# Performance work log

Hardware: AMD Instinct MI355X
Metric: run time of the kernel (lower is better)

The kernel has to match this reference:

```python
import jax, jax.numpy as jnp
import numpy as np

EPS = 1e-8  # torch cosine_similarity norm clamp

def _cos(a, b, axis=-1):
    na = jnp.maximum(jnp.linalg.norm(a, axis=axis), EPS)
    nb = jnp.maximum(jnp.linalg.norm(b, axis=axis), EPS)
    return jnp.sum(a * b, axis=axis) / (na * nb)

def setup_inputs() -> dict:
    key = jax.random.key(0)
    ks = jax.random.split(key, 9)
    B, L, D, S = 8, 8192, 512, 131072
    scale = 0.02
    x = jax.random.normal(ks[0], (B, L, D), jnp.float32)
    context_W = jax.random.normal(ks[1], (D, D), jnp.float32) * scale
    context_b = jnp.zeros((D,), jnp.float32)
    pred_W1 = jax.random.normal(ks[2], (D, D), jnp.float32) * scale
    pred_b1 = jnp.zeros((D,), jnp.float32)
    pred_W2 = jax.random.normal(ks[3], (D, D), jnp.float32) * scale
    pred_b2 = jnp.zeros((D,), jnp.float32)
    raw_embeddings = jax.random.normal(ks[4], (S, D), jnp.float32)
    u = jax.random.uniform(ks[5], (S,), jnp.float32)
    surprise_level = jnp.where(u > 0.5, u, 0.0)  # ~half the slots active
    return {"x": x, "context_W": context_W, "context_b": context_b,
            "pred_W1": pred_W1, "pred_b1": pred_b1,
            "pred_W2": pred_W2, "pred_b2": pred_b2,
            "raw_embeddings": raw_embeddings, "surprise_level": surprise_level}

def reference(x, context_W, context_b, pred_W1, pred_b1, pred_W2, pred_b2,
              raw_embeddings, surprise_level):
    # context = pad(x[:, :-1], left-shift by one along seq), i.e. causal previous token
    context = jnp.pad(x[:, :-1, :], ((0, 0), (1, 0), (0, 0)))
    # predictor MLP on projected context (torch Linear: y = x @ W.T + b)
    ctx = context @ context_W.T + context_b
    h = jax.nn.gelu(ctx @ pred_W1.T + pred_b1, approximate=False)
    prediction = h @ pred_W2.T + pred_b2  # [B, L, D]
    mse = jnp.mean((x - prediction) ** 2, axis=-1)
    prediction_surprise = jnp.sqrt(mse)  # [B, L]

    # memory-contrastive surprise: cosine sim of pooled x vs active stored embeddings
    active = surprise_level > 0  # [S]
    x_pooled = jnp.mean(x, axis=1)  # [B, D]
    sim = _cos(x_pooled[:, None, :], raw_embeddings[None, :, :])  # [B, S]
    sim = jnp.where(active[None, :], sim, -jnp.inf)
    max_sim = jnp.max(sim, axis=-1)           # [B]
    best_idx = jnp.argmax(sim, axis=-1)       # [B]
    best_stored = raw_embeddings[best_idx]    # [B, D] argmax-based gather
    divergence = 1.0 - _cos(x, best_stored[:, None, :])  # [B, L]
    pattern_match = (max_sim[:, None] > 0.3).astype(x.dtype)
    contrastive = pattern_match * divergence

    surprise = jnp.maximum(prediction_surprise, contrastive * 2.0)  # [B, L]
    return surprise
```

## Files before the change

### kernel.cpp

```cpp
#include <hip/hip_runtime.h>
#include <math.h>

#define OFF_SIMKEY   0
#define OFF_POOLED   1024
#define ZEROED_BYTES 17408
#define OFF_MAXSIM   17408
#define OFF_NORME    17664
#define OFF_EBEST    17920
#define OFF_BPRIME   34304
#define OFF_WP       36864
#define OFF_W2B      561152

typedef __attribute__((ext_vector_type(8))) short bf16x8;
typedef __attribute__((ext_vector_type(4))) float f32x4;

__device__ inline unsigned short f2bf(float f) {
    unsigned int u = __float_as_uint(f);
    unsigned int r = (u + 0x7FFFu + ((u >> 16) & 1u)) >> 16;
    return (unsigned short)r;
}

__global__ void __launch_bounds__(256) k_pre(const float* __restrict__ W1, const float* __restrict__ Wc,
                      const float* __restrict__ b1, const float* __restrict__ bc,
                      unsigned short* __restrict__ Wp, float* __restrict__ bprime) {
    __shared__ float w1row[512];
    __shared__ float wsum[4];
    int t = threadIdx.x;
    int n = blockIdx.x >> 1, half = blockIdx.x & 1;
    if (t < 128) ((float4*)w1row)[t] = ((const float4*)(W1 + (size_t)n * 512))[t];
    __syncthreads();
    int k = half * 256 + t;
    float acc = 0.f;
#pragma unroll 8
    for (int j = 0; j < 512; ++j) acc += w1row[j] * Wc[(size_t)j * 512 + k];
    Wp[(size_t)n * 512 + k] = f2bf(acc);
    if (half == 0) {
        float p = w1row[t] * bc[t] + w1row[t + 256] * bc[t + 256];
#pragma unroll
        for (int m = 32; m >= 1; m >>= 1) p += __shfl_xor(p, m);
        if ((t & 63) == 0) wsum[t >> 6] = p;
        __syncthreads();
        if (t == 0) bprime[n] = b1[n] + wsum[0] + wsum[1] + wsum[2] + wsum[3];
    }
}

__global__ void __launch_bounds__(256) k_cast(const float* __restrict__ W2, unsigned short* __restrict__ W2b) {
    int i = blockIdx.x * 1024 + threadIdx.x * 4;
    float4 v = *(const float4*)(W2 + i);
    ushort4 o;
    o.x = f2bf(v.x); o.y = f2bf(v.y); o.z = f2bf(v.z); o.w = f2bf(v.w);
    *(ushort4*)(W2b + i) = o;
}

__global__ void __launch_bounds__(512) k_pool(const float* __restrict__ x, float* __restrict__ pooled) {
    __shared__ float4 pb[4][128];
    int t = threadIdx.x;
    int q = t & 127;
    int rg = t >> 7;
    int b = blockIdx.y;
    int l0 = blockIdx.x * 128;
    const float4* p = (const float4*)(x + ((size_t)b * 8192 + l0 + rg) * 512) + q;
    float4 s = make_float4(0.f, 0.f, 0.f, 0.f);
#pragma unroll 8
    for (int i = 0; i < 32; ++i) {
        float4 v = p[(size_t)i * 512];
        s.x += v.x; s.y += v.y; s.z += v.z; s.w += v.w;
    }
    pb[rg][q] = s;
    __syncthreads();
    if (rg == 0) {
        float4 a = pb[0][q], b1_ = pb[1][q], c = pb[2][q], d = pb[3][q];
        atomicAdd(&pooled[b * 512 + q * 4 + 0], a.x + b1_.x + c.x + d.x);
        atomicAdd(&pooled[b * 512 + q * 4 + 1], a.y + b1_.y + c.y + d.y);
        atomicAdd(&pooled[b * 512 + q * 4 + 2], a.z + b1_.z + c.z + d.z);
        atomicAdd(&pooled[b * 512 + q * 4 + 3], a.w + b1_.w + c.w + d.w);
    }
}

__global__ void __launch_bounds__(256) k_sim(const float* __restrict__ E, const float* __restrict__ sl,
                     const float* __restrict__ pooledws, unsigned long long* __restrict__ simkey) {
    __shared__ float ps[4096];
    __shared__ unsigned long long wkey[4][8];
    int t = threadIdx.x, lane = t & 63, w = t >> 6;
#pragma unroll
    for (int c = 0; c < 16; ++c) ps[t + c * 256] = pooledws[t + c * 256] * (1.0f / 8192.0f);
    __syncthreads();
    float pr[8][8];
#pragma unroll
    for (int b = 0; b < 8; ++b) {
        float4 v0 = *(const float4*)&ps[b * 512 + lane * 8];
        float4 v1 = *(const float4*)&ps[b * 512 + lane * 8 + 4];
        pr[b][0] = v0.x; pr[b][1] = v0.y; pr[b][2] = v0.z; pr[b][3] = v0.w;
        pr[b][4] = v1.x; pr[b][5] = v1.y; pr[b][6] = v1.z; pr[b][7] = v1.w;
    }
    float npinv[8];
#pragma unroll
    for (int b = 0; b < 8; ++b) {
        float s = 0.f;
#pragma unroll
        for (int j = 0; j < 8; ++j) s += pr[b][j] * pr[b][j];
#pragma unroll
        for (int m = 32; m >= 1; m >>= 1) s += __shfl_xor(s, m);
        npinv[b] = 1.0f / fmaxf(sqrtf(s), 1e-8f);
    }
    unsigned long long best[8];
#pragma unroll
    for (int b = 0; b < 8; ++b) best[b] = 0ull;
    int sbase = blockIdx.x * 64 + w * 16;
    float mysl = (lane < 16) ? sl[sbase + lane] : 0.f;
    unsigned long long mask = __ballot(mysl > 0.0f);
    for (int it = 0; it < 16; ++it) {
        if (!((mask >> it) & 1ull)) continue;
        int s = sbase + it;
        const float4* ep = (const float4*)(E + (size_t)s * 512);
        float4 e0 = ep[lane * 2], e1 = ep[lane * 2 + 1];
        float nrm = e0.x * e0.x + e0.y * e0.y + e0.z * e0.z + e0.w * e0.w
                  + e1.x * e1.x + e1.y * e1.y + e1.z * e1.z + e1.w * e1.w;
        float dt[8];
#pragma unroll
        for (int b = 0; b < 8; ++b)
            dt[b] = e0.x * pr[b][0] + e0.y * pr[b][1] + e0.z * pr[b][2] + e0.w * pr[b][3]
                  + e1.x * pr[b][4] + e1.y * pr[b][5] + e1.z * pr[b][6] + e1.w * pr[b][7];
#pragma unroll
        for (int m = 32; m >= 1; m >>= 1) {
            nrm += __shfl_xor(nrm, m);
#pragma unroll
            for (int b = 0; b < 8; ++b) dt[b] += __shfl_xor(dt[b], m);
        }
        float neinv = 1.0f / fmaxf(sqrtf(nrm), 1e-8f);
#pragma unroll
        for (int b = 0; b < 8; ++b) {
            float sim = dt[b] * npinv[b] * neinv;
            unsigned int u = __float_as_uint(sim);
            unsigned int k32 = (u & 0x80000000u) ? ~u : (u | 0x80000000u);
            unsigned long long key = ((unsigned long long)k32 << 32) | (unsigned int)(~(unsigned int)s);
            if (key > best[b]) best[b] = key;
        }
    }
    if (lane == 0) {
#pragma unroll
        for (int b = 0; b < 8; ++b) wkey[w][b] = best[b];
    }
    __syncthreads();
    if (t < 8) {
        unsigned long long k = wkey[0][t];
#pragma unroll
        for (int w2 = 1; w2 < 4; ++w2) if (wkey[w2][t] > k) k = wkey[w2][t];
        if (k) atomicMax(&simkey[t], k);
    }
}

__global__ void __launch_bounds__(64) k_b2(const float* __restrict__ E, const unsigned long long* __restrict__ simkey,
                    float* __restrict__ max_sim, float* __restrict__ norm_e, float* __restrict__ ebest) {
    int b = blockIdx.x, lane = threadIdx.x;
    unsigned long long key = simkey[b];
    float ms; unsigned int idx;
    if (key == 0ull) { ms = -1e30f; idx = 0u; }
    else {
        unsigned int k32 = (unsigned int)(key >> 32);
        unsigned int u = (k32 & 0x80000000u) ? (k32 & 0x7FFFFFFFu) : ~k32;
        ms = __uint_as_float(u);
        idx = ~(unsigned int)(key & 0xFFFFFFFFull);
    }
    const float4* ep = (const float4*)(E + (size_t)idx * 512);
    float4 e0 = ep[lane * 2], e1 = ep[lane * 2 + 1];
    *(float4*)&ebest[b * 512 + lane * 8] = e0;
    *(float4*)&ebest[b * 512 + lane * 8 + 4] = e1;
    float s = e0.x * e0.x + e0.y * e0.y + e0.z * e0.z + e0.w * e0.w
            + e1.x * e1.x + e1.y * e1.y + e1.z * e1.z + e1.w * e1.w;
#pragma unroll
    for (int m = 32; m >= 1; m >>= 1) s += __shfl_xor(s, m);
    if (lane == 0) { max_sim[b] = ms; norm_e[b] = fmaxf(sqrtf(s), 1e-8f); }
}

__global__ void __launch_bounds__(512, 2) k_mega(
        const float* __restrict__ x, const unsigned short* __restrict__ Wp,
        const float* __restrict__ bprime, const unsigned short* __restrict__ W2b,
        const float* __restrict__ b2, const float* __restrict__ ebest,
        const float* __restrict__ max_sim, const float* __restrict__ norm_e,
        float* __restrict__ out) {
    __shared__ char smem[137216];
    unsigned int*   Ts32 = (unsigned int*)(smem);
    unsigned short* Ts   = (unsigned short*)(smem);
    unsigned short* Hs   = (unsigned short*)(smem + 65536);
    float*          red  = (float*)(smem + 131072);

    const int t = threadIdx.x;
    const int lane = t & 63, w = t >> 6;
    const int l15 = lane & 15, quad = lane >> 4;
    const int gr0 = blockIdx.x * 64;
    const int b = gr0 >> 13;

    const int r = t >> 3, cc = t & 7;
    const int sR = (r >> 1) & 3;
    const int d0 = (((cc >> 2) ^ sR) << 2) | (cc & 3);
    const int d1 = ((((cc >> 2) + 2) ^ sR) << 2) | (cc & 3);

    int tsoff[4], hoff[4];
#pragma unroll
    for (int i = 0; i < 4; ++i) {
        int rowA = i * 16 + l15;
        tsoff[i] = rowA * 32 + ((quad ^ ((rowA >> 1) & 3)) << 3);
        hoff[i]  = rowA * 32 + ((quad ^ ((rowA >> 2) & 3)) << 3);
    }

    const unsigned short* bp1[4];
    const unsigned short* bp2[4];
#pragma unroll
    for (int j = 0; j < 4; ++j) {
        int n = w * 64 + j * 16 + l15;
        bp1[j] = Wp  + n * 512 + quad * 8;
        bp2[j] = W2b + n * 512 + quad * 8;
    }

    {
        int gr = gr0 + r;
        bool z = ((gr & 8191) == 0);
        const float* src = x + ((size_t)gr - 1) * 512 + cc * 2;
#pragma unroll
        for (int kt = 0; kt < 16; ++kt) {
            float2 v0 = make_float2(0.f, 0.f), v1 = make_float2(0.f, 0.f);
            if (!z) { v0 = *(const float2*)(src + kt * 32); v1 = *(const float2*)(src + kt * 32 + 16); }
            Ts32[kt * 1024 + r * 16 + d0] = (unsigned int)f2bf(v0.x) | ((unsigned int)f2bf(v0.y) << 16);
            Ts32[kt * 1024 + r * 16 + d1] = (unsigned int)f2bf(v1.x) | ((unsigned int)f2bf(v1.y) << 16);
        }
    }
    __syncthreads();

    f32x4 acc[4][4];
#pragma unroll
    for (int i = 0; i < 4; ++i)
#pragma unroll
        for (int j = 0; j < 4; ++j) acc[i][j] = (f32x4){0.f, 0.f, 0.f, 0.f};
#pragma unroll
    for (int kt = 0; kt < 16; ++kt) {
        bf16x8 af[4], bfr[4];
#pragma unroll
        for (int i = 0; i < 4; ++i) af[i] = *(const bf16x8*)&Ts[kt * 2048 + tsoff[i]];
#pragma unroll
        for (int j = 0; j < 4; ++j) bfr[j] = *(const bf16x8*)(bp1[j] + kt * 32);
#pragma unroll
        for (int i = 0; i < 4; ++i)
#pragma unroll
            for (int j = 0; j < 4; ++j)
                acc[i][j] = __builtin_amdgcn_mfma_f32_16x16x32_bf16(af[i], bfr[j], acc[i][j], 0, 0, 0);
    }

    {
        float bpj[4];
#pragma unroll
        for (int j = 0; j < 4; ++j) bpj[j] = bprime[w * 64 + j * 16 + l15];
#pragma unroll
        for (int i = 0; i < 4; ++i)
#pragma unroll
            for (int j = 0; j < 4; ++j)
#pragma unroll
                for (int rg = 0; rg < 4; ++rg) {
                    int m = i * 16 + quad * 4 + rg;
                    int ktc = w * 2 + (j >> 1);
                    int grp = ((j & 1) * 2 + (l15 >> 3)) ^ ((m >> 2) & 3);
                    float v = acc[i][j][rg] + bpj[j];
                    v = 0.5f * v * (1.0f + erff(v * 0.70710678118f));
                    Hs[ktc * 2048 + m * 32 + grp * 8 + (l15 & 7)] = f2bf(v);
                }
    }
    __syncthreads();

    f32x4 acc2[4][4];
#pragma unroll
    for (int i = 0; i < 4; ++i)
#pragma unroll
        for (int j = 0; j < 4; ++j) acc2[i][j] = (f32x4){0.f, 0.f, 0.f, 0.f};
#pragma unroll
    for (int kt = 0; kt < 16; ++kt) {
        bf16x8 af[4], bfr[4];
#pragma unroll
        for (int i = 0; i < 4; ++i) af[i] = *(const bf16x8*)&Hs[kt * 2048 + hoff[i]];
#pragma unroll
        for (int j = 0; j < 4; ++j) bfr[j] = *(const bf16x8*)(bp2[j] + kt * 32);
#pragma unroll
        for (int i = 0; i < 4; ++i)
#pragma unroll
            for (int j = 0; j < 4; ++j)
                acc2[i][j] = __builtin_amdgcn_mfma_f32_16x16x32_bf16(af[i], bfr[j], acc2[i][j], 0, 0, 0);
    }

    {
        float b2j[4], ej[4];
#pragma unroll
        for (int j = 0; j < 4; ++j) {
            int n = w * 64 + j * 16 + l15;
            b2j[j] = b2[n];
            ej[j] = ebest[b * 512 + n];
        }
#pragma unroll
        for (int i = 0; i < 4; ++i)
#pragma unroll
            for (int rg = 0; rg < 4; ++rg) {
                int m = i * 16 + quad * 4 + rg;
                int gr = gr0 + m;
                float sd = 0.f, sx = 0.f, sdt = 0.f;
#pragma unroll
                for (int j = 0; j < 4; ++j) {
                    int n = w * 64 + j * 16 + l15;
                    float p = acc2[i][j][rg] + b2j[j];
                    float xv = x[(size_t)gr * 512 + n];
                    float d = xv - p;
                    sd += d * d; sx += xv * xv; sdt += xv * ej[j];
                }
#pragma unroll
                for (int mm = 8; mm >= 1; mm >>= 1) {
                    sd += __shfl_xor(sd, mm);
                    sx += __shfl_xor(sx, mm);
                    sdt += __shfl_xor(sdt, mm);
                }
                if (l15 == 0) {
                    red[(m * 8 + w) * 3 + 0] = sd;
                    red[(m * 8 + w) * 3 + 1] = sx;
                    red[(m * 8 + w) * 3 + 2] = sdt;
                }
            }
    }
    __syncthreads();
    if (t < 64) {
        float sd = 0.f, sx = 0.f, sdt = 0.f;
#pragma unroll
        for (int w2 = 0; w2 < 8; ++w2) {
            sd  += red[(t * 8 + w2) * 3 + 0];
            sx  += red[(t * 8 + w2) * 3 + 1];
            sdt += red[(t * 8 + w2) * 3 + 2];
        }
        float ps = sqrtf(sd * (1.0f / 512.0f));
        float ms = max_sim[b];
        float c = 0.f;
        if (ms > 0.3f) {
            float nx = fmaxf(sqrtf(sx), 1e-8f);
            c = 2.0f * (1.0f - sdt / (nx * norm_e[b]));
        }
        out[gr0 + t] = fmaxf(ps, c);
    }
}

extern "C" void kernel_launch(void* const* d_in, const int* in_sizes, int n_in,
                              void* d_out, int out_size, void* d_ws, size_t ws_size,
                              hipStream_t stream) {
    const float* x  = (const float*)d_in[0];
    const float* Wc = (const float*)d_in[1];
    const float* bc = (const float*)d_in[2];
    const float* W1 = (const float*)d_in[3];
    const float* b1 = (const float*)d_in[4];
    const float* W2 = (const float*)d_in[5];
    const float* b2 = (const float*)d_in[6];
    const float* E  = (const float*)d_in[7];
    const float* sl = (const float*)d_in[8];

    char* ws = (char*)d_ws;
    unsigned long long* simkey = (unsigned long long*)(ws + OFF_SIMKEY);
    float* pooled  = (float*)(ws + OFF_POOLED);
    float* max_sim = (float*)(ws + OFF_MAXSIM);
    float* norm_e  = (float*)(ws + OFF_NORME);
    float* ebest   = (float*)(ws + OFF_EBEST);
    float* bprime  = (float*)(ws + OFF_BPRIME);
    unsigned short* Wp  = (unsigned short*)(ws + OFF_WP);
    unsigned short* W2b = (unsigned short*)(ws + OFF_W2B);
    float* out = (float*)d_out;

    hipMemsetAsync(ws, 0, ZEROED_BYTES, stream);
    k_pre<<<1024, 256, 0, stream>>>(W1, Wc, b1, bc, Wp, bprime);
    k_cast<<<256, 256, 0, stream>>>(W2, W2b);
    k_pool<<<dim3(64, 8), 512, 0, stream>>>(x, pooled);
    k_sim<<<2048, 256, 0, stream>>>(E, sl, pooled, simkey);
    k_b2<<<8, 64, 0, stream>>>(E, simkey, max_sim, norm_e, ebest);
    k_mega<<<1024, 512, 0, stream>>>(x, Wp, bprime, W2b, b2, ebest, max_sim, norm_e, out);
}
```

Measured before the change: 695.8 us.

## Alias hidden tile onto input tile and prefetch weight fragments to double occupancy

```diff
diff --git a/kernel.cpp b/kernel.cpp
--- a/kernel.cpp
+++ b/kernel.cpp
@@ -173,17 +173,17 @@
     if (lane == 0) { max_sim[b] = ms; norm_e[b] = fmaxf(sqrtf(s), 1e-8f); }
 }
 
-__global__ void __launch_bounds__(512, 2) k_mega(
+__global__ void __launch_bounds__(512, 4) k_mega(
         const float* __restrict__ x, const unsigned short* __restrict__ Wp,
         const float* __restrict__ bprime, const unsigned short* __restrict__ W2b,
         const float* __restrict__ b2, const float* __restrict__ ebest,
         const float* __restrict__ max_sim, const float* __restrict__ norm_e,
         float* __restrict__ out) {
-    __shared__ char smem[137216];
+    __shared__ char smem[71680];
     unsigned int*   Ts32 = (unsigned int*)(smem);
     unsigned short* Ts   = (unsigned short*)(smem);
-    unsigned short* Hs   = (unsigned short*)(smem + 65536);
-    float*          red  = (float*)(smem + 131072);
+    unsigned short* Hs   = (unsigned short*)(smem);
+    float*          red  = (float*)(smem + 65536);
 
     const int t = threadIdx.x;
     const int lane = t & 63, w = t >> 6;
@@ -232,19 +232,29 @@
     for (int i = 0; i < 4; ++i)
 #pragma unroll
         for (int j = 0; j < 4; ++j) acc[i][j] = (f32x4){0.f, 0.f, 0.f, 0.f};
-#pragma unroll
-    for (int kt = 0; kt < 16; ++kt) {
-        bf16x8 af[4], bfr[4];
-#pragma unroll
-        for (int i = 0; i < 4; ++i) af[i] = *(const bf16x8*)&Ts[kt * 2048 + tsoff[i]];
-#pragma unroll
-        for (int j = 0; j < 4; ++j) bfr[j] = *(const bf16x8*)(bp1[j] + kt * 32);
-#pragma unroll
-        for (int i = 0; i < 4; ++i)
-#pragma unroll
-            for (int j = 0; j < 4; ++j)
-                acc[i][j] = __builtin_amdgcn_mfma_f32_16x16x32_bf16(af[i], bfr[j], acc[i][j], 0, 0, 0);
-    }
+    {
+        bf16x8 bcur[4], bnxt[4];
+#pragma unroll
+        for (int j = 0; j < 4; ++j) bcur[j] = *(const bf16x8*)(bp1[j]);
+#pragma unroll
+        for (int kt = 0; kt < 16; ++kt) {
+            if (kt < 15) {
+#pragma unroll
+                for (int j = 0; j < 4; ++j) bnxt[j] = *(const bf16x8*)(bp1[j] + (kt + 1) * 32);
+            }
+            bf16x8 af[4];
+#pragma unroll
+            for (int i = 0; i < 4; ++i) af[i] = *(const bf16x8*)&Ts[kt * 2048 + tsoff[i]];
+#pragma unroll
+            for (int i = 0; i < 4; ++i)
+#pragma unroll
+                for (int j = 0; j < 4; ++j)
+                    acc[i][j] = __builtin_amdgcn_mfma_f32_16x16x32_bf16(af[i], bcur[j], acc[i][j], 0, 0, 0);
+#pragma unroll
+            for (int j = 0; j < 4; ++j) bcur[j] = bnxt[j];
+        }
+    }
+    __syncthreads();
 
     {
         float bpj[4];
@@ -271,18 +281,27 @@
     for (int i = 0; i < 4; ++i)
 #pragma unroll
         for (int j = 0; j < 4; ++j) acc2[i][j] = (f32x4){0.f, 0.f, 0.f, 0.f};
-#pragma unroll
-    for (int kt = 0; kt < 16; ++kt) {
-        bf16x8 af[4], bfr[4];
-#pragma unroll
-        for (int i = 0; i < 4; ++i) af[i] = *(const bf16x8*)&Hs[kt * 2048 + hoff[i]];
-#pragma unroll
-        for (int j = 0; j < 4; ++j) bfr[j] = *(const bf16x8*)(bp2[j] + kt * 32);
-#pragma unroll
-        for (int i = 0; i < 4; ++i)
-#pragma unroll
-            for (int j = 0; j < 4; ++j)
-                acc2[i][j] = __builtin_amdgcn_mfma_f32_16x16x32_bf16(af[i], bfr[j], acc2[i][j], 0, 0, 0);
+    {
+        bf16x8 bcur[4], bnxt[4];
+#pragma unroll
+        for (int j = 0; j < 4; ++j) bcur[j] = *(const bf16x8*)(bp2[j]);
+#pragma unroll
+        for (int kt = 0; kt < 16; ++kt) {
+            if (kt < 15) {
+#pragma unroll
+                for (int j = 0; j < 4; ++j) bnxt[j] = *(const bf16x8*)(bp2[j] + (kt + 1) * 32);
+            }
+            bf16x8 af[4];
+#pragma unroll
+            for (int i = 0; i < 4; ++i) af[i] = *(const bf16x8*)&Hs[kt * 2048 + hoff[i]];
+#pragma unroll
+            for (int i = 0; i < 4; ++i)
+#pragma unroll
+                for (int j = 0; j < 4; ++j)
+                    acc2[i][j] = __builtin_amdgcn_mfma_f32_16x16x32_bf16(af[i], bcur[j], acc2[i][j], 0, 0, 0);
+#pragma unroll
+            for (int j = 0; j < 4; ++j) bcur[j] = bnxt[j];
+        }
     }
 
     {
```

Result: faster. 667.8 us (-4.0%).
